# Performance work log

Hardware: AMD Instinct MI355X
Metric: run time of the kernel (lower is better)

The kernel has to match this reference:

```python
import jax, jax.numpy as jnp
import numpy as np

T, B, H = 1024, 128, 256


def setup_inputs() -> dict:
    key = jax.random.key(0)
    k1, k2, k3, k4, k5 = jax.random.split(key, 5)
    ins = jax.random.normal(k1, (T, B, H), dtype=jnp.float32)
    resets = jax.random.randint(k2, (T, B), 0, 2).astype(jnp.bool_)
    # GRUCell params (flax layout): input dense (with bias) and recurrent dense
    # (bias only on the candidate 'hn' branch). Orthogonal-ish init approximated
    # by scaled normal for a pure-jnp reference.
    s = 1.0 / np.sqrt(H)
    Wi = jax.random.normal(k3, (H, 3 * H), dtype=jnp.float32) * s   # -> [ir|iz|in]
    Wh = jax.random.normal(k4, (H, 3 * H), dtype=jnp.float32) * s   # -> [hr|hz|hn]
    bi = jnp.zeros((3 * H,), dtype=jnp.float32)
    bhn = jnp.zeros((H,), dtype=jnp.float32)
    h0 = jnp.zeros((B, H), dtype=jnp.float32)  # initialize_carry -> zeros
    return {"ins": ins, "resets": resets, "h0": h0,
            "Wi": Wi, "Wh": Wh, "bi": bi, "bhn": bhn}


def reference(ins, resets, h0, Wi, Wh, bi, bhn):
    """ScannedRNN: GRU recurrence over time with per-step reset masking.

    ins: [T,B,H], resets: [T,B] bool, h0: [B,H]. Returns (final_carry, ys).
    """
    Hh = h0.shape[-1]

    def step(h, xt):
        x_t, r_t = xt                              # [B,H], [B]
        h = jnp.where(r_t[:, None], 0.0, h)        # reset carry to zeros
        gi = x_t @ Wi + bi                         # [B,3H]
        gh = h @ Wh                                # [B,3H]
        i_r, i_z, i_n = gi[:, :Hh], gi[:, Hh:2 * Hh], gi[:, 2 * Hh:]
        h_r, h_z, h_n = gh[:, :Hh], gh[:, Hh:2 * Hh], gh[:, 2 * Hh:]
        r = jax.nn.sigmoid(i_r + h_r)
        z = jax.nn.sigmoid(i_z + h_z)
        n = jnp.tanh(i_n + r * (h_n + bhn))
        h_new = (1.0 - z) * n + z * h
        return h_new, h_new                        # GRUCell returns (carry, y=carry)

    h_final, ys = jax.lax.scan(step, h0, (ins, resets))
    return h_final, ys
```

## Files before the change

kernel.cpp:

```cpp
#include <hip/hip_runtime.h>


typedef _Float16 half2_t __attribute__((ext_vector_type(2)));
typedef _Float16 half4_t __attribute__((ext_vector_type(4)));
typedef _Float16 half8_t __attribute__((ext_vector_type(8)));
typedef float f32x4 __attribute__((ext_vector_type(4)));

#define T_DIM 1024
#define B_DIM 128
#define H_DIM 256
#define N3 768
#define NSTREAM 4096
#define ROWS 16

__device__ __forceinline__ int perm_n(int cp) {
  int ublk = cp / 48;
  int rem = cp % 48;
  int g = rem >> 4;
  int u4 = rem & 15;
  return g * 256 + ublk * 16 + u4;
}


__global__ void prep_whb(const float* __restrict__ Wh, unsigned* __restrict__ WhB) {
  int i = blockIdx.x * 256 + threadIdx.x;
  int h = 2 * i;
  int idx = h & 7;
  int lane = (h >> 3) & 63;
  int ntk = h >> 9;
  int nt = ntk % 48;
  int kt = ntk / 48;
  int k = kt * 32 + ((lane >> 4) * 8) + idx;
  int n = perm_n(nt * 16 + (lane & 15));
  half2_t p;
  p.x = (_Float16)Wh[(size_t)k * N3 + n];
  p.y = (_Float16)Wh[(size_t)(k + 1) * N3 + n];
  WhB[i] = __builtin_bit_cast(unsigned, p);
}

__global__ void prep_witp(const float* __restrict__ Wi, _Float16* __restrict__ WiTp) {
  int i = blockIdx.x * 256 + threadIdx.x;
  int cp = i >> 8;
  int k = i & 255;
  WiTp[(size_t)cp * 256 + k] = (_Float16)Wi[(size_t)k * N3 + perm_n(cp)];
}

__global__ void prep_bip(const float* __restrict__ bi, float* __restrict__ bip) {
  int i = threadIdx.x;
  bip[i] = bi[perm_n(i)];
}

__global__ void init_h(const float* __restrict__ h0, float* __restrict__ h_state) {
  int i = blockIdx.x * 256 + threadIdx.x;
  h_state[i] = h0[i];
}

__global__ __launch_bounds__(256) void conv_a(
    const float* __restrict__ src, _Float16* __restrict__ dst, int n8) {
  int i = blockIdx.x * 256 + threadIdx.x;
  const int stride = gridDim.x * 256;
  for (; i < n8; i += stride) {
    float4 a = ((const float4*)src)[2 * i];
    float4 b = ((const float4*)src)[2 * i + 1];
    half8_t h;
    h[0] = (_Float16)a.x; h[1] = (_Float16)a.y;
    h[2] = (_Float16)a.z; h[3] = (_Float16)a.w;
    h[4] = (_Float16)b.x; h[5] = (_Float16)b.y;
    h[6] = (_Float16)b.z; h[7] = (_Float16)b.w;
    ((half8_t*)dst)[i] = h;
  }
}


__global__ void seg_transpose(const int* __restrict__ resets, int* __restrict__ resT) {
  int i = blockIdx.x * 256 + threadIdx.x;
  int b = i >> 10;
  int t = i & 1023;
  resT[i] = resets[(size_t)t * B_DIM + b];
}

__global__ __launch_bounds__(256) void seg_extract(
    const int* __restrict__ resT, int t0, int steps,
    unsigned* __restrict__ rowsegs, unsigned* __restrict__ rowcnt,
    unsigned* __restrict__ lhist) {
  const int b = blockIdx.x;
  const int tid = threadIdx.x;
  const int lane = tid & 63;
  const int w = tid >> 6;
  const int per = (steps + 255) >> 8;

  __shared__ unsigned short sstartL[1025];
  __shared__ unsigned lcur[1025];
  __shared__ unsigned wsum[4];

  for (int l = tid; l <= steps; l += 256) lcur[l] = 0;

  const int* rrow = resT + (size_t)b * T_DIM + t0;
  int myfirst = tid * per;
  unsigned cnt = 0;
  for (int i = 0; i < per; ++i) {
    int s = myfirst + i;
    if (s < steps && (s == 0 || rrow[s] != 0)) cnt++;
  }
  unsigned pre = cnt;
#pragma unroll
  for (int off = 1; off < 64; off <<= 1) {
    unsigned v = __shfl_up(pre, off);
    if (lane >= off) pre += v;
  }
  if (lane == 63) wsum[w] = pre;
  __syncthreads();
  unsigned wbase = 0, total = 0;
#pragma unroll
  for (int i = 0; i < 4; ++i) {
    if (i < w) wbase += wsum[i];
    total += wsum[i];
  }
  unsigned r = wbase + pre - cnt;
  for (int i = 0; i < per; ++i) {
    int s = myfirst + i;
    if (s < steps && (s == 0 || rrow[s] != 0)) sstartL[r++] = (unsigned short)s;
  }
  if (tid == 0) { sstartL[total] = (unsigned short)steps; rowcnt[b] = total; }
  __syncthreads();

  const unsigned carry0 = (rrow[0] == 0) ? 1u : 0u;
  for (unsigned rr = tid; rr < total; rr += 256) {
    int st = sstartL[rr];
    int len = (int)sstartL[rr + 1] - st;
    unsigned carry = (st == 0) ? carry0 : 0u;
    unsigned rk = atomicAdd(&lcur[len], 1u);
    rowsegs[(size_t)b * T_DIM + rr] =
        (unsigned)st | ((unsigned)len << 10) | (rk << 21) | (carry << 31);
  }
  __syncthreads();
  for (int l = tid; l <= steps; l += 256) lhist[(size_t)l * 128 + b] = lcur[l];
}

__global__ __launch_bounds__(1024) void seg_prefix2(
    const unsigned* __restrict__ lhist, unsigned* __restrict__ rowoff,
    unsigned* __restrict__ cursors, unsigned* __restrict__ Warr,
    unsigned* __restrict__ nseg, int steps) {
  __shared__ unsigned cs[1024];
  __shared__ unsigned cs2[1024];
  const int tid = threadIdx.x;
  const int len = tid + 1;
  unsigned run = 0;
  if (len <= steps) {
    for (int b = 0; b < 128; ++b) {
      rowoff[(size_t)len * 128 + b] = run;
      run += lhist[(size_t)len * 128 + b];
    }
  }
  unsigned own = run;
  unsigned own2 = run * (unsigned)len;
  cs[tid] = own;
  cs2[tid] = own2;
  for (int off = 1; off < 1024; off <<= 1) {
    __syncthreads();
    unsigned v = (tid + off < 1024) ? cs[tid + off] : 0u;
    unsigned v2 = (tid + off < 1024) ? cs2[tid + off] : 0u;
    __syncthreads();
    cs[tid] += v;
    cs2[tid] += v2;
  }
  cursors[len] = cs[tid] - own;
  Warr[len] = cs2[tid] - own2;
  if (tid == 0) *nseg = cs[0];
}

__global__ void seg_scatter2(
    const unsigned* __restrict__ rowsegs, const unsigned* __restrict__ rowcnt,
    const unsigned* __restrict__ rowoff, const unsigned* __restrict__ cursors,
    unsigned* __restrict__ segs) {
  int i = blockIdx.x * 256 + threadIdx.x;
  int b = i >> 10;
  int rr = i & 1023;
  if ((unsigned)rr >= rowcnt[b]) return;
  unsigned rec = rowsegs[i];
  unsigned st = rec & 0x3FF;
  unsigned len = (rec >> 10) & 0x7FF;
  unsigned rk = (rec >> 21) & 0x3FF;
  unsigned carry = rec >> 31;
  unsigned dst = cursors[len] + rowoff[(size_t)len * 128 + b] + rk;
  segs[dst] = st | (len << 10) | ((unsigned)b << 21) | (carry << 28);
}

__global__ void str_mark(
    const unsigned* __restrict__ segs, const unsigned* __restrict__ nseg_p,
    const unsigned* __restrict__ cursors, const unsigned* __restrict__ Warr,
    unsigned* __restrict__ sstart, unsigned* __restrict__ preexS, int Q) {
  unsigned r = blockIdx.x * 256 + threadIdx.x;
  unsigned n = *nseg_p;
  if (r >= n) return;
  unsigned rec = segs[r];
  unsigned len = (rec >> 10) & 0x7FF;
  unsigned pre = Warr[len] + len * (r - cursors[len]);
  unsigned st = pre / (unsigned)Q;
  unsigned stp;
  if (r == 0) {
    sstart[0] = 0; preexS[0] = 0; stp = 0;
  } else {
    unsigned rec2 = segs[r - 1];
    unsigned len2 = (rec2 >> 10) & 0x7FF;
    unsigned pre2 = Warr[len2] + len2 * (r - 1 - cursors[len2]);
    stp = pre2 / (unsigned)Q;
  }
  for (unsigned s = stp + 1; s <= st; ++s) { sstart[s] = r; preexS[s] = pre; }
}

__global__ __launch_bounds__(256) void gi_gemm(
    const _Float16* __restrict__ A16,
    const _Float16* __restrict__ BT,
    const float* __restrict__ bip,
    _Float16* __restrict__ Cout,
    int M) {
  __shared__ _Float16 Al[128 * 32];
  __shared__ _Float16 Bl[128 * 32];
  const int tid = threadIdx.x;
  const int lane = tid & 63;
  const int w = tid >> 6;
  const int wr = w >> 1, wc = w & 1;
  const int m0 = blockIdx.y * 128;
  const int n0 = blockIdx.x * 128;

  const int srow = lane >> 2;
  const int schunk = lane & 3;

  f32x4 acc[4][4] = {};

  for (int ks = 0; ks < 256; ks += 32) {
#pragma unroll
    for (int rr = 0; rr < 2; ++rr) {
      const int row = w * 32 + rr * 16;
      __builtin_amdgcn_global_load_lds(
          (const __attribute__((address_space(1))) void*)
              ((const char*)A16 + ((size_t)(m0 + row + srow) * 256 + ks) * 2 + schunk * 16),
          (__attribute__((address_space(3))) void*)((char*)Al + row * 64),
          16, 0, 0);
      __builtin_amdgcn_global_load_lds(
          (const __attribute__((address_space(1))) void*)
              ((const char*)BT + ((size_t)(n0 + row + srow) * 256 + ks) * 2 + schunk * 16),
          (__attribute__((address_space(3))) void*)((char*)Bl + row * 64),
          16, 0, 0);
    }
    __syncthreads();

    half8_t af[4], bf[4];
#pragma unroll
    for (int m = 0; m < 4; ++m)
      af[m] = *(const half8_t*)&Al[(size_t)(wr * 64 + m * 16 + (lane & 15)) * 32 + (lane >> 4) * 8];
#pragma unroll
    for (int n = 0; n < 4; ++n)
      bf[n] = *(const half8_t*)&Bl[(size_t)(wc * 64 + n * 16 + (lane & 15)) * 32 + (lane >> 4) * 8];
#pragma unroll
    for (int m = 0; m < 4; ++m)
#pragma unroll
      for (int n = 0; n < 4; ++n)
        acc[m][n] = __builtin_amdgcn_mfma_f32_16x16x32_f16(af[m], bf[n], acc[m][n], 0, 0, 0);
    __syncthreads();
  }

#pragma unroll
  for (int m = 0; m < 4; ++m) {
    int row = m0 + wr * 64 + m * 16 + (lane >> 4) * 4;
#pragma unroll
    for (int n = 0; n < 4; ++n) {
      int col = n0 + wc * 64 + n * 16 + (lane & 15);
      float bv = bip[col];
#pragma unroll
      for (int r2 = 0; r2 < 4; ++r2)
        Cout[(size_t)(row + r2) * N3 + col] = (_Float16)(acc[m][n][r2] + bv);
    }
  }
}

__global__ __launch_bounds__(512)
__attribute__((amdgpu_waves_per_eu(1, 2)))
void scan_stream(
    const _Float16* __restrict__ WhB,
    const _Float16* __restrict__ gi,
    const unsigned* __restrict__ segs,
    const unsigned* __restrict__ sstart,
    const unsigned* __restrict__ preexS,
    const unsigned* __restrict__ nseg_ptr,
    const float* __restrict__ bhn,
    const float* __restrict__ h_in,
    float* __restrict__ h_out,
    float* __restrict__ ys,
    float* __restrict__ hfin,
    float* __restrict__ dump,
    int t0, int steps, int Q) {
  __shared__ _Float16 h_lds[2][ROWS][264];
  __shared__ _Float16 giL[2][ROWS][776];
  __shared__ unsigned rst[ROWS];
  __shared__ unsigned rowrankL[ROWS];
  __shared__ unsigned rowpwL[ROWS];
  __shared__ unsigned wava[8];

  const int tid = threadIdx.x;
  const int lane = tid & 63;
  const int w = tid >> 6;
  const int sbase = blockIdx.x * ROWS;
  const unsigned nseg = *nseg_ptr;
  float* dumpb = dump + (size_t)(blockIdx.x & 63) * 4096;

  if (tid < ROWS) {
    const unsigned st = sbase + tid;
    unsigned r = sstart[st], pw = preexS[st];
    unsigned v = 0u, rk = 0xFFFFFFFFu, rpw0 = 0u;
    if (r < nseg && pw < (st + 1) * (unsigned)Q) {
      unsigned rec = segs[r];
      unsigned len = (rec >> 10) & 0x7FF;
      v = (rec & 0x3FF) | (((rec >> 21) & 0x7F) << 10) | (len << 17) |
          (((rec >> 28) & 1u) << 28);
      rk = r; rpw0 = pw + len;
    }
    rst[tid] = v; rowrankL[tid] = rk; rowpwL[tid] = rpw0;
  }
  if (tid < 8) wava[tid] = 1u;

  half8_t whr[48];
#pragma unroll
  for (int kt = 0; kt < 8; ++kt)
#pragma unroll
    for (int q = 0; q < 6; ++q)
      whr[kt * 6 + q] =
          *(const half8_t*)&WhB[(((size_t)kt * 48 + w * 6 + q) * 64 + lane) * 8];

  __syncthreads();

  unsigned rcur[2], rnxt[2], rrk[2], rpw[2], segnx[2], lim[2];
  unsigned rfr[2];
  float4 hfresh[2];
#pragma unroll
  for (int rr = 0; rr < 2; ++rr) {
    const int row = 2 * w + rr;
    rcur[rr] = rst[row];
    rrk[rr]  = rowrankL[row];
    rpw[rr]  = rowpwL[row];
    lim[rr]  = (unsigned)(sbase + row + 1) * (unsigned)Q;
    unsigned rn2 = rrk[rr] + 1;
    unsigned i2 = (rn2 < nseg) ? rn2 : (nseg - 1);
    segnx[rr] = segs[i2];
  }

#pragma unroll
  for (int rr = 0; rr < 2; ++rr) {
    int row = 2 * w + rr;
    unsigned s = rcur[rr];
    float4 o = make_float4(0.f, 0.f, 0.f, 0.f);
    if (s & (1u << 28))
      o = *(const float4*)&h_in[(size_t)((s >> 10) & 0x7F) * 256 + lane * 4];
    half4_t hv;
    hv.x = (_Float16)o.x; hv.y = (_Float16)o.y;
    hv.z = (_Float16)o.z; hv.w = (_Float16)o.w;
    *(half4_t*)&h_lds[0][row][lane * 4] = hv;
  }

#pragma unroll
  for (int rr = 0; rr < 2; ++rr) {
    const int row = 2 * w + rr;
    const unsigned ss = rcur[rr];
    const int live = (int)((ss >> 17) & 0x7FF);
    const size_t goff = live ? ((size_t)(ss & 0x3FF) * B_DIM + ((ss >> 10) & 0x7F)) * N3 : 0;
    const char* src = (const char*)(gi + goff);
    char* dst = (char*)&giL[0][row][0];
    __builtin_amdgcn_global_load_lds(
        (const __attribute__((address_space(1))) void*)(src + (size_t)lane * 16),
        (__attribute__((address_space(3))) void*)dst, 16, 0, 0);
    __builtin_amdgcn_global_load_lds(
        (const __attribute__((address_space(1))) void*)(src + 1024 + (size_t)lane * 4),
        (__attribute__((address_space(3))) void*)(dst + 1024), 4, 0, 0);
    __builtin_amdgcn_global_load_lds(
        (const __attribute__((address_space(1))) void*)(src + 1280 + (size_t)lane * 4),
        (__attribute__((address_space(3))) void*)(dst + 1280), 4, 0, 0);
  }
#pragma unroll
  for (int rr = 0; rr < 2; ++rr) {
    const int row = 2 * w + rr;
    *(float4*)&dumpb[row * 256 + lane * 4] = make_float4(0.f, 0.f, 0.f, 0.f);
  }

  const int r16 = lane & 15;
  const int q4 = (lane >> 4) * 4;
  const int kq8 = (lane >> 4) * 8;
  const int u0 = w * 32 + r16;
  const float bh0 = bhn[u0];
  const float bh1 = bhn[u0 + 16];

  int cur = 0;
  int hc = 0;
  while (true) {
    asm volatile("s_waitcnt vmcnt(2)" ::: "memory");
    asm volatile("s_waitcnt lgkmcnt(0)" ::: "memory");
    __builtin_amdgcn_s_barrier();
    __builtin_amdgcn_sched_barrier(0);

    unsigned alive = 0;
#pragma unroll
    for (int i = 0; i < 8; ++i) alive += wava[i];
    if (!alive) break;

#pragma unroll
    for (int rr = 0; rr < 2; ++rr) {
      const unsigned cs = rcur[rr];
      const unsigned rem = (cs >> 17) & 0x7FF;
      unsigned nx = 0u;
      rfr[rr] = 0u;
      if (rem > 1) {
        nx = ((cs & 0x3FF) + 1) | (cs & (0x7Fu << 10)) | ((rem - 1) << 17);
      } else if (rem == 1) {
        unsigned rn = rrk[rr] + 1;
        unsigned pw = rpw[rr];
        if (rn < nseg && pw < lim[rr]) {
          unsigned rec = segnx[rr];
          unsigned len = (rec >> 10) & 0x7FF;
          nx = (rec & 0x3FF) | (((rec >> 21) & 0x7F) << 10) | (len << 17) |
               (((rec >> 28) & 1u) << 28);
          rrk[rr] = rn; rpw[rr] = pw + len;
          rfr[rr] = 1u;
          unsigned rn2 = rn + 1;
          unsigned i2 = (rn2 < nseg) ? rn2 : (nseg - 1);
          segnx[rr] = segs[i2];
        }
      }
      rnxt[rr] = nx;
      hfresh[rr] = make_float4(0.f, 0.f, 0.f, 0.f);
      if (rfr[rr] && (nx & (1u << 28)))
        hfresh[rr] = *(const float4*)&h_in[(size_t)((nx >> 10) & 0x7F) * 256 + lane * 4];
    }

#pragma unroll
    for (int rr = 0; rr < 2; ++rr) {
      const int row = 2 * w + rr;
      const unsigned ss = rnxt[rr];
      const int live = (int)((ss >> 17) & 0x7FF);
      const size_t goff = live ? ((size_t)(ss & 0x3FF) * B_DIM + ((ss >> 10) & 0x7F)) * N3 : 0;
      const char* src = (const char*)(gi + goff);
      char* dst = (char*)&giL[cur ^ 1][row][0];
      __builtin_amdgcn_global_load_lds(
          (const __attribute__((address_space(1))) void*)(src + (size_t)lane * 16),
          (__attribute__((address_space(3))) void*)dst, 16, 0, 0);
      __builtin_amdgcn_global_load_lds(
          (const __attribute__((address_space(1))) void*)(src + 1024 + (size_t)lane * 4),
          (__attribute__((address_space(3))) void*)(dst + 1024), 4, 0, 0);
      __builtin_amdgcn_global_load_lds(
          (const __attribute__((address_space(1))) void*)(src + 1280 + (size_t)lane * 4),
          (__attribute__((address_space(3))) void*)(dst + 1280), 4, 0, 0);
    }

    f32x4 acc[6] = {};
#pragma unroll
    for (int kt = 0; kt < 8; ++kt) {
      half8_t afr = *(const half8_t*)&h_lds[hc][r16][kt * 32 + kq8];
#pragma unroll
      for (int q = 0; q < 6; ++q)
        acc[q] = __builtin_amdgcn_mfma_f32_16x16x32_f16(afr, whr[kt * 6 + q], acc[q], 0, 0, 0);
    }

    float gr[2][4], gz[2][4], gn[2][4], hold[2][4];
#pragma unroll
    for (int j = 0; j < 2; ++j) {
      const int u = u0 + j * 16;
      const int cb = w * 96 + j * 48 + r16;
#pragma unroll
      for (int e = 0; e < 4; ++e) {
        const int row = q4 + e;
        gr[j][e]   = (float)giL[cur][row][cb];
        gz[j][e]   = (float)giL[cur][row][cb + 16];
        gn[j][e]   = (float)giL[cur][row][cb + 32];
        hold[j][e] = (float)h_lds[hc][row][u];
      }
    }
#pragma unroll
    for (int j = 0; j < 2; ++j) {
      const int u = u0 + j * 16;
      const float bh = j ? bh1 : bh0;
#pragma unroll
      for (int e = 0; e < 4; ++e) {
        const int row = q4 + e;
        const float sigr = __builtin_amdgcn_rcpf(1.f + __expf(-(gr[j][e] + acc[3 * j][e])));
        const float sigz = __builtin_amdgcn_rcpf(1.f + __expf(-(gz[j][e] + acc[3 * j + 1][e])));
        const float narg = fmaf(sigr, acc[3 * j + 2][e] + bh, gn[j][e]);
        const float eo = __expf(-2.f * narg);
        const float nn = fmaf(2.f, __builtin_amdgcn_rcpf(1.f + eo), -1.f);
        const float hnew = fmaf(sigz, hold[j][e] - nn, nn);
        h_lds[hc ^ 1][row][u] = (_Float16)hnew;
      }
    }

    asm volatile("s_waitcnt lgkmcnt(0)" ::: "memory");
    __builtin_amdgcn_s_barrier();
    __builtin_amdgcn_sched_barrier(0);

    unsigned alv = 0;
#pragma unroll
    for (int rr = 0; rr < 2; ++rr) {
      const int row = 2 * w + rr;
      const unsigned sp = rcur[rr];
      const unsigned rem = (sp >> 17) & 0x7FF;
      const int t = sp & 0x3FF;
      const int b = (sp >> 10) & 0x7F;
      half4_t hv = *(const half4_t*)&h_lds[hc ^ 1][row][lane * 4];
      float4 o;
      o.x = (float)hv.x; o.y = (float)hv.y; o.z = (float)hv.z; o.w = (float)hv.w;
      float* ydst = rem
          ? &ys[(((size_t)(t0 + t) * B_DIM + b) * H_DIM) + lane * 4]
          : &dumpb[row * 256 + lane * 4];
      *(float4*)ydst = o;
      if (rem == 1) {
        if (t == steps - 1) *(float4*)&h_out[(size_t)b * 256 + lane * 4] = o;
        if (t0 + t == T_DIM - 1) *(float4*)&hfin[(size_t)b * 256 + lane * 4] = o;
      }
      if ((rnxt[rr] >> 17) & 0x7FF) alv++;
      rcur[rr] = rnxt[rr];
      if (rfr[rr]) {
        half4_t hv2;
        hv2.x = (_Float16)hfresh[rr].x; hv2.y = (_Float16)hfresh[rr].y;
        hv2.z = (_Float16)hfresh[rr].z; hv2.w = (_Float16)hfresh[rr].w;
        *(half4_t*)&h_lds[hc ^ 1][row][lane * 4] = hv2;
      }
    }
    if (lane == 0) wava[w] = alv;

    cur ^= 1;
    hc ^= 1;
  }
}

extern "C" void kernel_launch(void* const* d_in, const int* in_sizes, int n_in,
                              void* d_out, int out_size, void* d_ws, size_t ws_size,
                              hipStream_t stream) {
  const float* ins    = (const float*)d_in[0];
  const int*   resets = (const int*)d_in[1];
  const float* h0     = (const float*)d_in[2];
  const float* Wi     = (const float*)d_in[3];
  const float* Wh     = (const float*)d_in[4];
  const float* bi     = (const float*)d_in[5];
  const float* bhn    = (const float*)d_in[6];
  float* out  = (float*)d_out;
  float* hfin = out;
  float* ys   = out + B_DIM * H_DIM;

  char* ws = (char*)d_ws;
  unsigned*  WhB     = (unsigned*)(ws + 0);
  _Float16*  WiTp    = (_Float16*)(ws + 393216);
  float*     bip     = (float*)(ws + 786432);
  float*     hA      = (float*)(ws + 789504);
  float*     hB      = (float*)(ws + 920576);
  int*       resT    = (int*)(ws + 1051648);
  unsigned*  rowsegs = (unsigned*)(ws + 1575936);
  unsigned*  rowcnt  = (unsigned*)(ws + 2100224);
  unsigned*  lhist   = (unsigned*)(ws + 2100736);
  unsigned*  rowoff  = (unsigned*)(ws + 2625536);
  unsigned*  cursors = (unsigned*)(ws + 3150336);
  unsigned*  Warr    = (unsigned*)(ws + 3154560);
  unsigned*  nseg    = (unsigned*)(ws + 3158784);
  unsigned*  segs    = (unsigned*)(ws + 3158912);
  unsigned*  sstart  = (unsigned*)(ws + 3683200);
  unsigned*  preexS  = (unsigned*)(ws + 3748736);
  float*     dump    = (float*)(ws + 3814400);
  const size_t gi_off = 4862976;

  int CH = T_DIM;
  while (CH > 256) {
    size_t need = gi_off + (size_t)CH * 128 * (N3 + H_DIM) * 2;
    if (need <= ws_size) break;
    CH >>= 1;
  }
  _Float16* gibuf = (_Float16*)(ws + gi_off);
  _Float16* A16   = (_Float16*)(ws + gi_off + (size_t)CH * 128 * N3 * 2);

  prep_whb<<<384, 256, 0, stream>>>(Wh, WhB);
  prep_witp<<<768, 256, 0, stream>>>(Wi, WiTp);
  prep_bip<<<1, 768, 0, stream>>>(bi, bip);
  init_h<<<128, 256, 0, stream>>>(h0, hA);
  seg_transpose<<<512, 256, 0, stream>>>(resets, resT);

  float* hbufs[2] = {hA, hB};
  for (int c = 0, t0 = 0; t0 < T_DIM; ++c, t0 += CH) {
    int steps = (t0 + CH <= T_DIM) ? CH : (T_DIM - t0);
    int M = steps * B_DIM;
    int Q = (M + NSTREAM - 1) / NSTREAM;
    if (Q < 1) Q = 1;

    conv_a<<<2048, 256, 0, stream>>>(ins + (size_t)t0 * B_DIM * H_DIM, A16, M * 32);

    dim3 ggrid(N3 / 128, M / 128);
    gi_gemm<<<ggrid, 256, 0, stream>>>(A16, WiTp, bip, gibuf, M);

    seg_extract<<<128, 256, 0, stream>>>(resT, t0, steps, rowsegs, rowcnt, lhist);
    seg_prefix2<<<1, 1024, 0, stream>>>(lhist, rowoff, cursors, Warr, nseg, steps);
    seg_scatter2<<<512, 256, 0, stream>>>(rowsegs, rowcnt, rowoff, cursors, segs);
    hipMemsetAsync(sstart, 0xFF, 131072, stream);
    str_mark<<<512, 256, 0, stream>>>(segs, nseg, cursors, Warr, sstart, preexS, Q);

    scan_stream<<<NSTREAM / ROWS, 512, 0, stream>>>(
        (const _Float16*)WhB, gibuf, segs, sstart, preexS, nseg, bhn,
        hbufs[c & 1], hbufs[(c + 1) & 1], ys, hfin, dump, t0, steps, Q);
  }
}
```

Baseline: 448.3 us.

## Remove second per-step barrier by fusing output writes into gate epilogue

Each lane now writes its computed h values straight to ys/h_out/hfin in the gate epilogue. Previously every step ended with a second barrier and a row-wise LDS readback to do those writes. Row schedule records move into a triple-buffered LDS ring, one step ahead, so the gate lanes know each row's current and next segment. They also fetch fresh initial-state values for new segments themselves, and a ballot over the schedule replaces the wava liveness counter. This drops one barrier per timestep. In exchange, the global stores become scalar and scattered rather than float4 per lane, and the vmcnt wait threshold changes.

```diff
diff --git a/kernel.cpp b/kernel.cpp
--- a/kernel.cpp
+++ b/kernel.cpp
@@ -293,10 +293,9 @@
     int t0, int steps, int Q) {
   __shared__ _Float16 h_lds[2][ROWS][264];
   __shared__ _Float16 giL[2][ROWS][776];
-  __shared__ unsigned rst[ROWS];
+  __shared__ unsigned recL[3][ROWS];
   __shared__ unsigned rowrankL[ROWS];
   __shared__ unsigned rowpwL[ROWS];
-  __shared__ unsigned wava[8];
 
   const int tid = threadIdx.x;
   const int lane = tid & 63;
@@ -316,9 +315,8 @@
           (((rec >> 28) & 1u) << 28);
       rk = r; rpw0 = pw + len;
     }
-    rst[tid] = v; rowrankL[tid] = rk; rowpwL[tid] = rpw0;
-  }
-  if (tid < 8) wava[tid] = 1u;
+    recL[0][tid] = v; rowrankL[tid] = rk; rowpwL[tid] = rpw0;
+  }
 
   half8_t whr[48];
 #pragma unroll
@@ -330,57 +328,64 @@
 
   __syncthreads();
 
-  unsigned rcur[2], rnxt[2], rrk[2], rpw[2], segnx[2], lim[2];
-  unsigned rfr[2];
-  float4 hfresh[2];
+  unsigned rB[2], rrk[2], rpw[2], segnx[2], lim[2];
 #pragma unroll
   for (int rr = 0; rr < 2; ++rr) {
     const int row = 2 * w + rr;
-    rcur[rr] = rst[row];
-    rrk[rr]  = rowrankL[row];
-    rpw[rr]  = rowpwL[row];
-    lim[rr]  = (unsigned)(sbase + row + 1) * (unsigned)Q;
-    unsigned rn2 = rrk[rr] + 1;
-    unsigned i2 = (rn2 < nseg) ? rn2 : (nseg - 1);
+    const unsigned r0 = recL[0][row];
+    rrk[rr] = rowrankL[row];
+    rpw[rr] = rowpwL[row];
+    lim[rr] = (unsigned)(sbase + row + 1) * (unsigned)Q;
+    unsigned i2 = (rrk[rr] + 1 < nseg) ? rrk[rr] + 1 : (nseg - 1);
     segnx[rr] = segs[i2];
-  }
-
-#pragma unroll
-  for (int rr = 0; rr < 2; ++rr) {
-    int row = 2 * w + rr;
-    unsigned s = rcur[rr];
+
     float4 o = make_float4(0.f, 0.f, 0.f, 0.f);
-    if (s & (1u << 28))
-      o = *(const float4*)&h_in[(size_t)((s >> 10) & 0x7F) * 256 + lane * 4];
+    if (r0 & (1u << 28))
+      o = *(const float4*)&h_in[(size_t)((r0 >> 10) & 0x7F) * 256 + lane * 4];
     half4_t hv;
     hv.x = (_Float16)o.x; hv.y = (_Float16)o.y;
     hv.z = (_Float16)o.z; hv.w = (_Float16)o.w;
     *(half4_t*)&h_lds[0][row][lane * 4] = hv;
-  }
-
-#pragma unroll
-  for (int rr = 0; rr < 2; ++rr) {
-    const int row = 2 * w + rr;
-    const unsigned ss = rcur[rr];
-    const int live = (int)((ss >> 17) & 0x7FF);
-    const size_t goff = live ? ((size_t)(ss & 0x3FF) * B_DIM + ((ss >> 10) & 0x7F)) * N3 : 0;
-    const char* src = (const char*)(gi + goff);
-    char* dst = (char*)&giL[0][row][0];
-    __builtin_amdgcn_global_load_lds(
-        (const __attribute__((address_space(1))) void*)(src + (size_t)lane * 16),
-        (__attribute__((address_space(3))) void*)dst, 16, 0, 0);
-    __builtin_amdgcn_global_load_lds(
-        (const __attribute__((address_space(1))) void*)(src + 1024 + (size_t)lane * 4),
-        (__attribute__((address_space(3))) void*)(dst + 1024), 4, 0, 0);
-    __builtin_amdgcn_global_load_lds(
-        (const __attribute__((address_space(1))) void*)(src + 1280 + (size_t)lane * 4),
-        (__attribute__((address_space(3))) void*)(dst + 1280), 4, 0, 0);
-  }
-#pragma unroll
-  for (int rr = 0; rr < 2; ++rr) {
-    const int row = 2 * w + rr;
-    *(float4*)&dumpb[row * 256 + lane * 4] = make_float4(0.f, 0.f, 0.f, 0.f);
-  }
+
+    {
+      const int live = (int)((r0 >> 17) & 0x7FF);
+      const size_t goff = live ? ((size_t)(r0 & 0x3FF) * B_DIM + ((r0 >> 10) & 0x7F)) * N3 : 0;
+      const char* src = (const char*)(gi + goff);
+      char* dst = (char*)&giL[0][row][0];
+      __builtin_amdgcn_global_load_lds(
+          (const __attribute__((address_space(1))) void*)(src + (size_t)lane * 16),
+          (__attribute__((address_space(3))) void*)dst, 16, 0, 0);
+      __builtin_amdgcn_global_load_lds(
+          (const __attribute__((address_space(1))) void*)(src + 1024 + (size_t)lane * 4),
+          (__attribute__((address_space(3))) void*)(dst + 1024), 4, 0, 0);
+      __builtin_amdgcn_global_load_lds(
+          (const __attribute__((address_space(1))) void*)(src + 1280 + (size_t)lane * 4),
+          (__attribute__((address_space(3))) void*)(dst + 1280), 4, 0, 0);
+    }
+
+    unsigned cb = r0, nx = 0u;
+    {
+      unsigned rem = (cb >> 17) & 0x7FF;
+      if (rem > 1) {
+        nx = ((cb & 0x3FF) + 1) | (cb & (0x7Fu << 10)) | ((rem - 1) << 17);
+      } else if (rem == 1) {
+        unsigned rn = rrk[rr] + 1, pw = rpw[rr];
+        if (rn < nseg && pw < lim[rr]) {
+          unsigned rec = segnx[rr];
+          unsigned len = (rec >> 10) & 0x7FF;
+          nx = (rec & 0x3FF) | (((rec >> 21) & 0x7F) << 10) | (len << 17) |
+               (((rec >> 28) & 1u) << 28);
+          rrk[rr] = rn; rpw[rr] = pw + len;
+          unsigned j2 = (rn + 1 < nseg) ? rn + 1 : (nseg - 1);
+          segnx[rr] = segs[j2];
+        }
+      }
+    }
+    rB[rr] = nx;
+    if (lane == 0) recL[1][row] = nx;
+  }
+
+  __syncthreads();
 
   const int r16 = lane & 15;
   const int q4 = (lane >> 4) * 4;
@@ -389,52 +394,41 @@
   const float bh0 = bhn[u0];
   const float bh1 = bhn[u0 + 16];
 
+  int pa = 0, pb = 1, pc = 2;
   int cur = 0;
   int hc = 0;
   while (true) {
-    asm volatile("s_waitcnt vmcnt(2)" ::: "memory");
+    asm volatile("s_waitcnt vmcnt(8)" ::: "memory");
     asm volatile("s_waitcnt lgkmcnt(0)" ::: "memory");
     __builtin_amdgcn_s_barrier();
     __builtin_amdgcn_sched_barrier(0);
 
-    unsigned alive = 0;
-#pragma unroll
-    for (int i = 0; i < 8; ++i) alive += wava[i];
-    if (!alive) break;
-
-#pragma unroll
-    for (int rr = 0; rr < 2; ++rr) {
-      const unsigned cs = rcur[rr];
-      const unsigned rem = (cs >> 17) & 0x7FF;
-      unsigned nx = 0u;
-      rfr[rr] = 0u;
-      if (rem > 1) {
-        nx = ((cs & 0x3FF) + 1) | (cs & (0x7Fu << 10)) | ((rem - 1) << 17);
-      } else if (rem == 1) {
-        unsigned rn = rrk[rr] + 1;
-        unsigned pw = rpw[rr];
-        if (rn < nseg && pw < lim[rr]) {
-          unsigned rec = segnx[rr];
-          unsigned len = (rec >> 10) & 0x7FF;
-          nx = (rec & 0x3FF) | (((rec >> 21) & 0x7F) << 10) | (len << 17) |
-               (((rec >> 28) & 1u) << 28);
-          rrk[rr] = rn; rpw[rr] = pw + len;
-          rfr[rr] = 1u;
-          unsigned rn2 = rn + 1;
-          unsigned i2 = (rn2 < nseg) ? rn2 : (nseg - 1);
-          segnx[rr] = segs[i2];
-        }
+    unsigned rAv[4], rBv[4];
+#pragma unroll
+    for (int e = 0; e < 4; ++e) {
+      rAv[e] = recL[pa][q4 + e];
+      rBv[e] = recL[pb][q4 + e];
+    }
+    unsigned mliv = (rAv[0] | rAv[1] | rAv[2] | rAv[3]) & (0x7FFu << 17);
+    if (__ballot(mliv != 0) == 0ull) break;
+
+    float fr[2][4];
+#pragma unroll
+    for (int e = 0; e < 4; ++e) {
+      fr[0][e] = 0.f; fr[1][e] = 0.f;
+      const unsigned remA = (rAv[e] >> 17) & 0x7FF;
+      const unsigned rBe = rBv[e];
+      if (remA == 1 && ((rBe >> 17) & 0x7FF) && (rBe & (1u << 28))) {
+        const float* hb = &h_in[(size_t)((rBe >> 10) & 0x7F) * 256];
+        fr[0][e] = hb[u0];
+        fr[1][e] = hb[u0 + 16];
       }
-      rnxt[rr] = nx;
-      hfresh[rr] = make_float4(0.f, 0.f, 0.f, 0.f);
-      if (rfr[rr] && (nx & (1u << 28)))
-        hfresh[rr] = *(const float4*)&h_in[(size_t)((nx >> 10) & 0x7F) * 256 + lane * 4];
     }
 
 #pragma unroll
     for (int rr = 0; rr < 2; ++rr) {
       const int row = 2 * w + rr;
-      const unsigned ss = rnxt[rr];
+      const unsigned ss = rB[rr];
       const int live = (int)((ss >> 17) & 0x7FF);
       const size_t goff = live ? ((size_t)(ss & 0x3FF) * B_DIM + ((ss >> 10) & 0x7F)) * N3 : 0;
       const char* src = (const char*)(gi + goff);
@@ -480,50 +474,53 @@
 #pragma unroll
       for (int e = 0; e < 4; ++e) {
         const int row = q4 + e;
+        const unsigned rA = rAv[e];
+        const unsigned remA = (rA >> 17) & 0x7FF;
         const float sigr = __builtin_amdgcn_rcpf(1.f + __expf(-(gr[j][e] + acc[3 * j][e])));
         const float sigz = __builtin_amdgcn_rcpf(1.f + __expf(-(gz[j][e] + acc[3 * j + 1][e])));
         const float narg = fmaf(sigr, acc[3 * j + 2][e] + bh, gn[j][e]);
         const float eo = __expf(-2.f * narg);
         const float nn = fmaf(2.f, __builtin_amdgcn_rcpf(1.f + eo), -1.f);
         const float hnew = fmaf(sigz, hold[j][e] - nn, nn);
-        h_lds[hc ^ 1][row][u] = (_Float16)hnew;
+        const int t = rA & 0x3FF;
+        const int b = (rA >> 10) & 0x7F;
+        float* ydst = remA
+            ? &ys[(((size_t)(t0 + t) * B_DIM + b) * H_DIM) + u]
+            : &dumpb[row * 256 + u];
+        *ydst = hnew;
+        if (remA == 1) {
+          if (t == steps - 1) h_out[(size_t)b * 256 + u] = hnew;
+          if (t0 + t == T_DIM - 1) hfin[(size_t)b * 256 + u] = hnew;
+        }
+        const float hval = (remA > 1) ? hnew : fr[j][e];
+        h_lds[hc ^ 1][row][u] = (_Float16)hval;
       }
     }
 
-    asm volatile("s_waitcnt lgkmcnt(0)" ::: "memory");
-    __builtin_amdgcn_s_barrier();
-    __builtin_amdgcn_sched_barrier(0);
-
-    unsigned alv = 0;
 #pragma unroll
     for (int rr = 0; rr < 2; ++rr) {
-      const int row = 2 * w + rr;
-      const unsigned sp = rcur[rr];
-      const unsigned rem = (sp >> 17) & 0x7FF;
-      const int t = sp & 0x3FF;
-      const int b = (sp >> 10) & 0x7F;
-      half4_t hv = *(const half4_t*)&h_lds[hc ^ 1][row][lane * 4];
-      float4 o;
-      o.x = (float)hv.x; o.y = (float)hv.y; o.z = (float)hv.z; o.w = (float)hv.w;
-      float* ydst = rem
-          ? &ys[(((size_t)(t0 + t) * B_DIM + b) * H_DIM) + lane * 4]
-          : &dumpb[row * 256 + lane * 4];
-      *(float4*)ydst = o;
-      if (rem == 1) {
-        if (t == steps - 1) *(float4*)&h_out[(size_t)b * 256 + lane * 4] = o;
-        if (t0 + t == T_DIM - 1) *(float4*)&hfin[(size_t)b * 256 + lane * 4] = o;
+      const unsigned cb = rB[rr];
+      unsigned nx = 0u;
+      const unsigned rem = (cb >> 17) & 0x7FF;
+      if (rem > 1) {
+        nx = ((cb & 0x3FF) + 1) | (cb & (0x7Fu << 10)) | ((rem - 1) << 17);
+      } else if (rem == 1) {
+        unsigned rn = rrk[rr] + 1, pw = rpw[rr];
+        if (rn < nseg && pw < lim[rr]) {
+          unsigned rec = segnx[rr];
+          unsigned len = (rec >> 10) & 0x7FF;
+          nx = (rec & 0x3FF) | (((rec >> 21) & 0x7F) << 10) | (len << 17) |
+               (((rec >> 28) & 1u) << 28);
+          rrk[rr] = rn; rpw[rr] = pw + len;
+          unsigned j2 = (rn + 1 < nseg) ? rn + 1 : (nseg - 1);
+          segnx[rr] = segs[j2];
+        }
       }
-      if ((rnxt[rr] >> 17) & 0x7FF) alv++;
-      rcur[rr] = rnxt[rr];
-      if (rfr[rr]) {
-        half4_t hv2;
-        hv2.x = (_Float16)hfresh[rr].x; hv2.y = (_Float16)hfresh[rr].y;
-        hv2.z = (_Float16)hfresh[rr].z; hv2.w = (_Float16)hfresh[rr].w;
-        *(half4_t*)&h_lds[hc ^ 1][row][lane * 4] = hv2;
-      }
-    }
-    if (lane == 0) wava[w] = alv;
-
+      if (lane == 0) recL[pc][2 * w + rr] = nx;
+      rB[rr] = nx;
+    }
+
+    const int tp = pa; pa = pb; pb = pc; pc = tp;
     cur ^= 1;
     hc ^= 1;
   }
```

Result: slower. 543.2 us (+21.2%).
